# Kernel optimization log

Hardware: AMD Instinct MI355X
Metric: run time of the kernel (lower is better)

Reference implementation:

```python
import jax, jax.numpy as jnp
import numpy as np

HEAD_DIM = 128  # dim // num_heads; RoPE rot_dim and softmax scale
ROPE_THETA = 10000.0


def rope_rotate(x, rot_dim):
    # lucidrains RotaryEmbedding.rotate_queries_or_keys: rotate first rot_dim
    # channels of last axis with interleaved-pair rotation; pass rest through.
    T = x.shape[-2]
    inv_freq = 1.0 / (ROPE_THETA ** (jnp.arange(0, rot_dim, 2, dtype=jnp.float32) / rot_dim))
    freqs = jnp.arange(T, dtype=jnp.float32)[:, None] * inv_freq[None, :]  # [T, rot_dim//2]
    freqs = jnp.repeat(freqs, 2, axis=-1)  # [T, rot_dim] interleaved (f0,f0,f1,f1,...)
    cos, sin = jnp.cos(freqs), jnp.sin(freqs)
    xr, x_pass = x[..., :rot_dim], x[..., rot_dim:]
    x1, x2 = xr[..., 0::2], xr[..., 1::2]
    rot = jnp.stack([-x2, x1], axis=-1).reshape(xr.shape)  # rotate_half
    xr = xr * cos + rot * sin
    return jnp.concatenate([xr, x_pass], axis=-1)


def setup_inputs() -> dict:
    key = jax.random.key(0)
    ks = jax.random.split(key, 9)
    B, T, D = 2, 2048, 2048
    w = lambda k, shape: jax.random.normal(k, shape, dtype=jnp.float32) * 0.02
    return {
        "latent_space": jax.random.normal(ks[0], (B, T, D), dtype=jnp.float32),
        "Wq": w(ks[1], (D, D)), "bq": w(ks[2], (D,)),
        "Wk": w(ks[3], (D, D)), "bk": w(ks[4], (D,)),
        "Wv": w(ks[5], (D, D)), "bv": w(ks[6], (D,)),
        "Wfc": w(ks[7], (D, D)), "bfc": w(ks[8], (D,)),
    }


def reference(latent_space, Wq, bq, Wk, bk, Wv, bv, Wfc, bfc):
    # Projections (nn.Linear: x @ W.T + b)
    Q = latent_space @ Wq.T + bq
    K = latent_space @ Wk.T + bk
    V = latent_space @ Wv.T + bv
    # Fused RoPE on first HEAD_DIM channels (module never splits heads)
    Q = rope_rotate(Q, HEAD_DIM)
    K = rope_rotate(K, HEAD_DIM)
    # Full-hidden-dim QK^T: [B,T,T]
    qk = jnp.einsum('btd,bsd->bts', Q, K)
    T = qk.shape[-1]
    causal = jnp.triu(jnp.ones((T, T), dtype=bool), 1)
    A = jnp.where(causal, -jnp.inf, qk)
    # PartialSoftmax with temp=1, h_t=None: state = A/sqrt(head_dim);
    # out = exp(state)/sum(exp(state)) * 2
    state = A / jnp.sqrt(jnp.float32(HEAD_DIM))
    x_exp = jnp.exp(state)
    A = x_exp / jnp.sum(x_exp, axis=-1, keepdims=True) * 2.0
    out = jnp.einsum('bts,bsd->btd', A, V) @ Wfc.T + bfc
    return out
```

## Files before the change

### kernel.cpp

```cpp
#include <hip/hip_runtime.h>
#include <hip/hip_bf16.h>
#include <math.h>

using bf16 = __hip_bfloat16;
typedef __attribute__((ext_vector_type(8))) __bf16 bf16x8;
typedef __attribute__((ext_vector_type(4))) float f32x4;

static __device__ __forceinline__ void gload16(const bf16* g, bf16* l) {
  __builtin_amdgcn_global_load_lds((const __attribute__((address_space(1))) void*)g,
                                   (__attribute__((address_space(3))) void*)l, 16, 0, 0);
}

__global__ __launch_bounds__(256) void cvt_f32_bf16(const float* __restrict__ in,
                                                    bf16* __restrict__ out, int n4) {
  const int i = blockIdx.x * 256 + threadIdx.x;
  if (i >= n4) return;
  const float4 v = reinterpret_cast<const float4*>(in)[i];
  union { bf16 h[4]; short4 s; } u;
  u.h[0] = __float2bfloat16(v.x);
  u.h[1] = __float2bfloat16(v.y);
  u.h[2] = __float2bfloat16(v.z);
  u.h[3] = __float2bfloat16(v.w);
  *reinterpret_cast<short4*>(out + 4 * (size_t)i) = u.s;
}

template<bool BIAS, bool F32OUT, bool CAUSAL, bool KTRUNC>
__global__ __launch_bounds__(256, 2) void gemm_nt(
    const bf16* __restrict__ A, const bf16* __restrict__ B, void* __restrict__ Cv,
    const float* __restrict__ bias, int K, int lda, int ldb, int ldc,
    long sA, long sB, long sC)
{
  if (CAUSAL && blockIdx.x > blockIdx.y) return;
  A += (long)blockIdx.z * sA;
  B += (long)blockIdx.z * sB;
  const int rowBase = blockIdx.y * 128;
  const int colBase = blockIdx.x * 128;
  const int tid  = threadIdx.x;
  const int lane = tid & 63;
  const int wid  = tid >> 6;
  const int wR = (wid >> 1) * 64;
  const int wC = (wid & 1) * 64;

  __shared__ alignas(16) bf16 lsA[128 * 32];
  __shared__ alignas(16) bf16 lsB[128 * 32];

  f32x4 acc[4][4] = {};

  const int kEnd = KTRUNC ? (rowBase + 128) : K;
  const int rt = tid >> 2;
  const int c8 = (tid & 3) * 8;
  const bf16* gA = A + (size_t)(rowBase + rt) * lda + c8;
  const bf16* gB = B + (size_t)(colBase + rt) * ldb + c8;
  const int lr = lane >> 4;
  const int lc = lane & 15;

  for (int k0 = 0; k0 < kEnd; k0 += 32) {
    gload16(gA + k0,                    &lsA[rt * 32 + c8]);
    gload16(gA + (size_t)64 * lda + k0, &lsA[(rt + 64) * 32 + c8]);
    gload16(gB + k0,                    &lsB[rt * 32 + c8]);
    gload16(gB + (size_t)64 * ldb + k0, &lsB[(rt + 64) * 32 + c8]);
    __syncthreads();

    bf16x8 af[4], bf_[4];
#pragma unroll
    for (int m = 0; m < 4; ++m)
      af[m] = *reinterpret_cast<const bf16x8*>(&lsA[(wR + m * 16 + lc) * 32 + lr * 8]);
#pragma unroll
    for (int n = 0; n < 4; ++n)
      bf_[n] = *reinterpret_cast<const bf16x8*>(&lsB[(wC + n * 16 + lc) * 32 + lr * 8]);

#pragma unroll
    for (int m = 0; m < 4; ++m)
#pragma unroll
      for (int n = 0; n < 4; ++n)
        acc[m][n] = __builtin_amdgcn_mfma_f32_16x16x32_bf16(af[m], bf_[n], acc[m][n], 0, 0, 0);
    __syncthreads();
  }

  const long cbase = (long)blockIdx.z * sC;
#pragma unroll
  for (int m = 0; m < 4; ++m) {
    const int row0 = rowBase + wR + m * 16 + lr * 4;
#pragma unroll
    for (int n = 0; n < 4; ++n) {
      const int col = colBase + wC + n * 16 + lc;
      const float bv = BIAS ? bias[col] : 0.f;
#pragma unroll
      for (int j = 0; j < 4; ++j) {
        const float v = acc[m][n][j] + bv;
        const long idx = cbase + (long)(row0 + j) * ldc + col;
        if (F32OUT) reinterpret_cast<float*>(Cv)[idx] = v;
        else        reinterpret_cast<bf16*>(Cv)[idx] = __float2bfloat16(v);
      }
    }
  }
}

__global__ __launch_bounds__(256) void rope_bf16(bf16* __restrict__ X) {
  const int idx = blockIdx.x * 256 + threadIdx.x;
  const int row = idx >> 6;
  const int i   = idx & 63;
  const int t   = row & 2047;
  const float ang = (float)t * exp2f((float)i * -0.20762050593046f);
  float sn, cs;
  sincosf(ang, &sn, &cs);
  bf16* p = X + ((long)row << 11) + 2 * i;
  const float x1 = __bfloat162float(p[0]);
  const float x2 = __bfloat162float(p[1]);
  p[0] = __float2bfloat16(x1 * cs - x2 * sn);
  p[1] = __float2bfloat16(x2 * cs + x1 * sn);
}

__global__ __launch_bounds__(256) void softmax_causal(
    const float* __restrict__ S, bf16* __restrict__ Aout, long sS, long sA) {
  const int t = blockIdx.x;
  const int b = blockIdx.y;
  const float* row = S + (long)b * sS + (long)t * 2048;
  bf16* orow = Aout + (long)b * sA + (long)t * 4096;
  const int L = t + 1;
  __shared__ float e[2048];
  __shared__ float red[4];
  const float scale = 0.0883883476483184f;
  const int lane = threadIdx.x & 63, wd = threadIdx.x >> 6;

  float mx = -INFINITY;
  for (int s = threadIdx.x; s < L; s += 256) {
    const float v = row[s] * scale;
    e[s] = v;
    mx = fmaxf(mx, v);
  }
#pragma unroll
  for (int off = 1; off < 64; off <<= 1) mx = fmaxf(mx, __shfl_xor(mx, off));
  if (lane == 0) red[wd] = mx;
  __syncthreads();
  mx = fmaxf(fmaxf(red[0], red[1]), fmaxf(red[2], red[3]));
  __syncthreads();

  float sum = 0.f;
  for (int s = threadIdx.x; s < L; s += 256) {
    const float v = expf(e[s] - mx);
    e[s] = v;
    sum += v;
  }
#pragma unroll
  for (int off = 1; off < 64; off <<= 1) sum += __shfl_xor(sum, off);
  if (lane == 0) red[wd] = sum;
  __syncthreads();
  sum = red[0] + red[1] + red[2] + red[3];
  const float f = 2.f / sum;
  for (int s = threadIdx.x; s < 2048; s += 256) {
    const float v = (s < L) ? e[s] * f : 0.f;
    orow[s] = __float2bfloat16(v);
  }
}

__global__ __launch_bounds__(256) void transpose_bf16(
    const bf16* __restrict__ V, bf16* __restrict__ VT) {
  __shared__ bf16 tile[32][33];
  const long b = blockIdx.z;
  const int s0 = blockIdx.y * 32, d0 = blockIdx.x * 32;
  const int tx = threadIdx.x;
  const int ty = threadIdx.y;
  for (int i = ty; i < 32; i += 8)
    tile[i][tx] = V[(b * 2048 + s0 + i) * 2048 + d0 + tx];
  __syncthreads();
  for (int i = ty; i < 32; i += 8)
    VT[(b * 2048 + d0 + i) * 2048 + s0 + tx] = tile[tx][i];
}

extern "C" void kernel_launch(void* const* d_in, const int* in_sizes, int n_in,
                              void* d_out, int out_size, void* d_ws, size_t ws_size,
                              hipStream_t stream) {
  (void)in_sizes; (void)n_in; (void)out_size; (void)ws_size;
  const float* lat = (const float*)d_in[0];
  const float* Wq  = (const float*)d_in[1];
  const float* bq  = (const float*)d_in[2];
  const float* Wk  = (const float*)d_in[3];
  const float* bk  = (const float*)d_in[4];
  const float* Wv  = (const float*)d_in[5];
  const float* bv  = (const float*)d_in[6];
  const float* Wfc = (const float*)d_in[7];
  const float* bfc = (const float*)d_in[8];
  float* out = (float*)d_out;

  constexpr long T = 2048, D = 2048, MT = 4096;
  char* w = (char*)d_ws;
  bf16* latb = (bf16*)w;  w += MT * D * 2;
  bf16* wqb  = (bf16*)w;  w += D * D * 2;
  bf16* wkb  = (bf16*)w;  w += D * D * 2;
  bf16* wvb  = (bf16*)w;  w += D * D * 2;
  bf16* wfb  = (bf16*)w;  w += D * D * 2;
  bf16* Qb   = (bf16*)w;  w += MT * D * 2;
  bf16* Kb   = (bf16*)w;  w += MT * D * 2;
  bf16* Vb   = (bf16*)w;  w += MT * D * 2;
  bf16* VTb  = (bf16*)w;  w += MT * D * 2;
  float* S   = (float*)w; w += 2 * T * T * 4;
  bf16* Ab   = (bf16*)S;
  bf16* Ob   = latb;

  cvt_f32_bf16<<<8192, 256, 0, stream>>>(lat, latb, (int)(MT * D / 4));
  cvt_f32_bf16<<<4096, 256, 0, stream>>>(Wq, wqb, (int)(D * D / 4));
  cvt_f32_bf16<<<4096, 256, 0, stream>>>(Wk, wkb, (int)(D * D / 4));
  cvt_f32_bf16<<<4096, 256, 0, stream>>>(Wv, wvb, (int)(D * D / 4));
  cvt_f32_bf16<<<4096, 256, 0, stream>>>(Wfc, wfb, (int)(D * D / 4));

  dim3 g1(16, 32, 1);
  gemm_nt<true,false,false,false><<<g1, 256, 0, stream>>>(latb, wqb, Qb, bq, 2048, 2048, 2048, 2048, 0, 0, 0);
  gemm_nt<true,false,false,false><<<g1, 256, 0, stream>>>(latb, wkb, Kb, bk, 2048, 2048, 2048, 2048, 0, 0, 0);
  gemm_nt<true,false,false,false><<<g1, 256, 0, stream>>>(latb, wvb, Vb, bv, 2048, 2048, 2048, 2048, 0, 0, 0);

  rope_bf16<<<1024, 256, 0, stream>>>(Qb);
  rope_bf16<<<1024, 256, 0, stream>>>(Kb);

  dim3 g2(16, 16, 2);
  gemm_nt<false,true,true,false><<<g2, 256, 0, stream>>>(Qb, Kb, S, nullptr,
      2048, 2048, 2048, 2048, T * D, T * D, T * T);

  softmax_causal<<<dim3(2048, 2), 256, 0, stream>>>(S, Ab, T * T, T * 2 * T);

  transpose_bf16<<<dim3(64, 64, 2), dim3(32, 8), 0, stream>>>(Vb, VTb);

  gemm_nt<false,false,false,true><<<g2, 256, 0, stream>>>(Ab, VTb, Ob, nullptr,
      2048, 4096, 2048, 2048, T * 2 * T, D * T, T * D);

  gemm_nt<true,true,false,false><<<g1, 256, 0, stream>>>(Ob, wfb, out, bfc,
      2048, 2048, 2048, 2048, 0, 0, 0);
}
```

Measured before the change: 346.7 us.

## Batch launches, split-K QK^T, swizzle LDS, and reverse causal PV row order

```diff
diff --git a/kernel.cpp b/kernel.cpp
--- a/kernel.cpp
+++ b/kernel.cpp
@@ -11,29 +11,34 @@
                                    (__attribute__((address_space(3))) void*)l, 16, 0, 0);
 }
 
-__global__ __launch_bounds__(256) void cvt_f32_bf16(const float* __restrict__ in,
-                                                    bf16* __restrict__ out, int n4) {
+struct POff { long a[4]; long b[4]; long c[4]; const float* bias[4]; };
+struct CvtP { const float* s[5]; bf16* d[5]; int n4[5]; };
+
+__global__ __launch_bounds__(256) void cvt_f32_bf16(CvtP p) {
+  const int y = blockIdx.y;
   const int i = blockIdx.x * 256 + threadIdx.x;
-  if (i >= n4) return;
-  const float4 v = reinterpret_cast<const float4*>(in)[i];
-  union { bf16 h[4]; short4 s; } u;
+  if (i >= p.n4[y]) return;
+  const float4 v = reinterpret_cast<const float4*>(p.s[y])[i];
+  union { bf16 h[4]; short4 s4; } u;
   u.h[0] = __float2bfloat16(v.x);
   u.h[1] = __float2bfloat16(v.y);
   u.h[2] = __float2bfloat16(v.z);
   u.h[3] = __float2bfloat16(v.w);
-  *reinterpret_cast<short4*>(out + 4 * (size_t)i) = u.s;
+  *reinterpret_cast<short4*>(p.d[y] + 4 * (size_t)i) = u.s4;
 }
 
 template<bool BIAS, bool F32OUT, bool CAUSAL, bool KTRUNC>
-__global__ __launch_bounds__(256, 2) void gemm_nt(
-    const bf16* __restrict__ A, const bf16* __restrict__ B, void* __restrict__ Cv,
-    const float* __restrict__ bias, int K, int lda, int ldb, int ldc,
-    long sA, long sB, long sC)
+__global__ __launch_bounds__(256, 4) void gemm_nt(
+    const bf16* __restrict__ A, const bf16* __restrict__ B, char* __restrict__ Cv,
+    POff P, int K, int lda, int ldb, int ldc)
 {
   if (CAUSAL && blockIdx.x > blockIdx.y) return;
-  A += (long)blockIdx.z * sA;
-  B += (long)blockIdx.z * sB;
-  const int rowBase = blockIdx.y * 128;
+  const int z = blockIdx.z;
+  A = (const bf16*)((const char*)A + P.a[z]);
+  B = (const bf16*)((const char*)B + P.b[z]);
+  char* C = Cv + P.c[z];
+  const int by = KTRUNC ? (gridDim.y - 1 - blockIdx.y) : blockIdx.y;
+  const int rowBase = by * 128;
   const int colBase = blockIdx.x * 128;
   const int tid  = threadIdx.x;
   const int lane = tid & 63;
@@ -48,26 +53,28 @@
 
   const int kEnd = KTRUNC ? (rowBase + 128) : K;
   const int rt = tid >> 2;
-  const int c8 = (tid & 3) * 8;
-  const bf16* gA = A + (size_t)(rowBase + rt) * lda + c8;
-  const bf16* gB = B + (size_t)(colBase + rt) * ldb + c8;
+  const int cs = tid & 3;
+  const int srcOff = (cs ^ ((rt >> 1) & 3)) * 8;
+  const bf16* gA = A + (size_t)(rowBase + rt) * lda + srcOff;
+  const bf16* gB = B + (size_t)(colBase + rt) * ldb + srcOff;
   const int lr = lane >> 4;
   const int lc = lane & 15;
+  const int kb = (lr ^ ((lc >> 1) & 3)) * 8;
 
   for (int k0 = 0; k0 < kEnd; k0 += 32) {
-    gload16(gA + k0,                    &lsA[rt * 32 + c8]);
-    gload16(gA + (size_t)64 * lda + k0, &lsA[(rt + 64) * 32 + c8]);
-    gload16(gB + k0,                    &lsB[rt * 32 + c8]);
-    gload16(gB + (size_t)64 * ldb + k0, &lsB[(rt + 64) * 32 + c8]);
+    gload16(gA + k0,                    &lsA[tid * 8]);
+    gload16(gA + (size_t)64 * lda + k0, &lsA[2048 + tid * 8]);
+    gload16(gB + k0,                    &lsB[tid * 8]);
+    gload16(gB + (size_t)64 * ldb + k0, &lsB[2048 + tid * 8]);
     __syncthreads();
 
     bf16x8 af[4], bf_[4];
 #pragma unroll
     for (int m = 0; m < 4; ++m)
-      af[m] = *reinterpret_cast<const bf16x8*>(&lsA[(wR + m * 16 + lc) * 32 + lr * 8]);
+      af[m] = *reinterpret_cast<const bf16x8*>(&lsA[(wR + m * 16 + lc) * 32 + kb]);
 #pragma unroll
     for (int n = 0; n < 4; ++n)
-      bf_[n] = *reinterpret_cast<const bf16x8*>(&lsB[(wC + n * 16 + lc) * 32 + lr * 8]);
+      bf_[n] = *reinterpret_cast<const bf16x8*>(&lsB[(wC + n * 16 + lc) * 32 + kb]);
 
 #pragma unroll
     for (int m = 0; m < 4; ++m)
@@ -77,7 +84,7 @@
     __syncthreads();
   }
 
-  const long cbase = (long)blockIdx.z * sC;
+  const float* bias = P.bias[z];
 #pragma unroll
   for (int m = 0; m < 4; ++m) {
     const int row0 = rowBase + wR + m * 16 + lr * 4;
@@ -88,9 +95,9 @@
 #pragma unroll
       for (int j = 0; j < 4; ++j) {
         const float v = acc[m][n][j] + bv;
-        const long idx = cbase + (long)(row0 + j) * ldc + col;
-        if (F32OUT) reinterpret_cast<float*>(Cv)[idx] = v;
-        else        reinterpret_cast<bf16*>(Cv)[idx] = __float2bfloat16(v);
+        const long idx = (long)(row0 + j) * ldc + col;
+        if (F32OUT) reinterpret_cast<float*>(C)[idx] = v;
+        else        reinterpret_cast<bf16*>(C)[idx] = __float2bfloat16(v);
       }
     }
   }
@@ -112,11 +119,14 @@
 }
 
 __global__ __launch_bounds__(256) void softmax_causal(
-    const float* __restrict__ S, bf16* __restrict__ Aout, long sS, long sA) {
+    const float* __restrict__ S0, const float* __restrict__ S1,
+    const float* __restrict__ S2, const float* __restrict__ S3,
+    bf16* __restrict__ A0, bf16* __restrict__ A1) {
   const int t = blockIdx.x;
   const int b = blockIdx.y;
-  const float* row = S + (long)b * sS + (long)t * 2048;
-  bf16* orow = Aout + (long)b * sA + (long)t * 4096;
+  const float* ra = (b ? S2 : S0) + (long)t * 2048;
+  const float* rb = (b ? S3 : S1) + (long)t * 2048;
+  bf16* orow = (b ? A1 : A0) + (long)t * 4096;
   const int L = t + 1;
   __shared__ float e[2048];
   __shared__ float red[4];
@@ -125,7 +135,7 @@
 
   float mx = -INFINITY;
   for (int s = threadIdx.x; s < L; s += 256) {
-    const float v = row[s] * scale;
+    const float v = (ra[s] + rb[s]) * scale;
     e[s] = v;
     mx = fmaxf(mx, v);
   }
@@ -184,6 +194,7 @@
   float* out = (float*)d_out;
 
   constexpr long T = 2048, D = 2048, MT = 4096;
+  constexpr long TTB = T * T * 4;
   char* w = (char*)d_ws;
   bf16* latb = (bf16*)w;  w += MT * D * 2;
   bf16* wqb  = (bf16*)w;  w += D * D * 2;
@@ -194,35 +205,59 @@
   bf16* Kb   = (bf16*)w;  w += MT * D * 2;
   bf16* Vb   = (bf16*)w;  w += MT * D * 2;
   bf16* VTb  = (bf16*)w;  w += MT * D * 2;
-  float* S   = (float*)w; w += 2 * T * T * 4;
-  bf16* Ab   = (bf16*)S;
+  float* S0  = (float*)w; w += TTB;
+  float* S1  = (float*)w; w += TTB;
+  float* S2  = (float*)d_out;
+  float* S3  = (float*)((char*)d_out + TTB);
+  bf16* A0   = (bf16*)S0;
+  bf16* A1   = (bf16*)S3;
   bf16* Ob   = latb;
 
-  cvt_f32_bf16<<<8192, 256, 0, stream>>>(lat, latb, (int)(MT * D / 4));
-  cvt_f32_bf16<<<4096, 256, 0, stream>>>(Wq, wqb, (int)(D * D / 4));
-  cvt_f32_bf16<<<4096, 256, 0, stream>>>(Wk, wkb, (int)(D * D / 4));
-  cvt_f32_bf16<<<4096, 256, 0, stream>>>(Wv, wvb, (int)(D * D / 4));
-  cvt_f32_bf16<<<4096, 256, 0, stream>>>(Wfc, wfb, (int)(D * D / 4));
-
-  dim3 g1(16, 32, 1);
-  gemm_nt<true,false,false,false><<<g1, 256, 0, stream>>>(latb, wqb, Qb, bq, 2048, 2048, 2048, 2048, 0, 0, 0);
-  gemm_nt<true,false,false,false><<<g1, 256, 0, stream>>>(latb, wkb, Kb, bk, 2048, 2048, 2048, 2048, 0, 0, 0);
-  gemm_nt<true,false,false,false><<<g1, 256, 0, stream>>>(latb, wvb, Vb, bv, 2048, 2048, 2048, 2048, 0, 0, 0);
-
-  rope_bf16<<<1024, 256, 0, stream>>>(Qb);
-  rope_bf16<<<1024, 256, 0, stream>>>(Kb);
-
-  dim3 g2(16, 16, 2);
-  gemm_nt<false,true,true,false><<<g2, 256, 0, stream>>>(Qb, Kb, S, nullptr,
-      2048, 2048, 2048, 2048, T * D, T * D, T * T);
-
-  softmax_causal<<<dim3(2048, 2), 256, 0, stream>>>(S, Ab, T * T, T * 2 * T);
+  CvtP cp;
+  cp.s[0] = lat; cp.d[0] = latb; cp.n4[0] = (int)(MT * D / 4);
+  cp.s[1] = Wq;  cp.d[1] = wqb;  cp.n4[1] = (int)(D * D / 4);
+  cp.s[2] = Wk;  cp.d[2] = wkb;  cp.n4[2] = (int)(D * D / 4);
+  cp.s[3] = Wv;  cp.d[3] = wvb;  cp.n4[3] = (int)(D * D / 4);
+  cp.s[4] = Wfc; cp.d[4] = wfb;  cp.n4[4] = (int)(D * D / 4);
+  cvt_f32_bf16<<<dim3(8192, 5), 256, 0, stream>>>(cp);
+
+  POff pq = {};
+  for (int z = 0; z < 3; ++z) {
+    pq.a[z] = 0;
+    pq.b[z] = (long)z * D * D * 2;
+    pq.c[z] = (long)z * MT * D * 2;
+  }
+  pq.bias[0] = bq; pq.bias[1] = bk; pq.bias[2] = bv;
+  gemm_nt<true,false,false,false><<<dim3(16, 32, 3), 256, 0, stream>>>(
+      latb, wqb, (char*)Qb, pq, 2048, 2048, 2048, 2048);
+
+  rope_bf16<<<2048, 256, 0, stream>>>(Qb);
+
+  POff ps = {};
+  for (int z = 0; z < 4; ++z) {
+    ps.a[z] = (long)(z >> 1) * T * D * 2 + (long)(z & 1) * 1024 * 2;
+    ps.b[z] = ps.a[z];
+  }
+  ps.c[0] = 0;
+  ps.c[1] = TTB;
+  ps.c[2] = (char*)S2 - (char*)S0;
+  ps.c[3] = (char*)S3 - (char*)S0;
+  gemm_nt<false,true,true,false><<<dim3(16, 16, 4), 256, 0, stream>>>(
+      Qb, Kb, (char*)S0, ps, 1024, 2048, 2048, 2048);
+
+  softmax_causal<<<dim3(2048, 2), 256, 0, stream>>>(S0, S1, S2, S3, A0, A1);
 
   transpose_bf16<<<dim3(64, 64, 2), dim3(32, 8), 0, stream>>>(Vb, VTb);
 
-  gemm_nt<false,false,false,true><<<g2, 256, 0, stream>>>(Ab, VTb, Ob, nullptr,
-      2048, 4096, 2048, 2048, T * 2 * T, D * T, T * D);
-
-  gemm_nt<true,true,false,false><<<g1, 256, 0, stream>>>(Ob, wfb, out, bfc,
-      2048, 2048, 2048, 2048, 0, 0, 0);
-}
+  POff pv = {};
+  pv.a[0] = 0; pv.a[1] = (char*)A1 - (char*)A0;
+  pv.b[0] = 0; pv.b[1] = (long)D * T * 2;
+  pv.c[0] = 0; pv.c[1] = (long)T * D * 2;
+  gemm_nt<false,false,false,true><<<dim3(16, 16, 2), 256, 0, stream>>>(
+      (const bf16*)A0, VTb, (char*)Ob, pv, 2048, 4096, 2048, 2048);
+
+  POff pf = {};
+  pf.bias[0] = bfc;
+  gemm_nt<true,true,false,false><<<dim3(16, 32, 1), 256, 0, stream>>>(
+      Ob, wfb, (char*)out, pf, 2048, 2048, 2048, 2048);
+}
```

Result: faster. 313.5 us (-9.6%).
